# Kernel tuning notes

Measured on AMD Instinct MI355X. Metric: run time of the kernel, lower is better.

The kernel has to match this reference:

```python
import jax, jax.numpy as jnp
import numpy as np

N_NODES = 100000
N_EDGES = 1600000
D = 64
NUM_GROUPS = 2


def setup_inputs() -> dict:
    key = jax.random.key(0)
    k_h, k_ws, k_wg, k_src, k_dst, k_grp = jax.random.split(key, 6)
    h = jax.random.normal(k_h, (N_NODES, D), dtype=jnp.float32)
    # nn.Linear(in, out, bias=False) weights have shape [out, in]
    W_self = jax.random.normal(k_ws, (D, D), dtype=jnp.float32) * (1.0 / np.sqrt(D))
    W_groups = jax.random.normal(k_wg, (NUM_GROUPS, D, D), dtype=jnp.float32) * (1.0 / np.sqrt(D))
    src = jax.random.randint(k_src, (N_EDGES,), 0, N_NODES, dtype=jnp.int32)
    dst = jax.random.randint(k_dst, (N_EDGES,), 0, N_NODES, dtype=jnp.int32)
    group_labels = jax.random.randint(k_grp, (N_NODES,), 0, NUM_GROUPS, dtype=jnp.int32)
    return {"h": h, "W_self": W_self, "W_groups": W_groups,
            "src": src, "dst": dst, "group_labels": group_labels}


def reference(h, W_self, W_groups, src, dst, group_labels):
    # h: [N, d_in]; W_self: [d_out, d_in]; W_groups: [G, d_out, d_in]
    # Edge list (src, dst) replaces the DGL graph; message m_e = h[src_e],
    # transformed by W_groups[group[src_e]], scatter-added into dst_e.
    n_nodes = h.shape[0]
    num_groups = W_groups.shape[0]

    h_self = h @ W_self.T                       # [N, d_out]

    h_src = jnp.take(h, src, axis=0)            # [E, d_in] edge gather
    g_src = jnp.take(group_labels, src, axis=0)  # [E]

    h_agg = jnp.zeros((n_nodes, W_groups.shape[1]), dtype=h.dtype)
    for i in range(num_groups):  # small fixed loop over groups
        masked = jnp.where((g_src == i)[:, None], h_src, 0.0)  # [E, d_in]
        # Linearity lets us aggregate first, then transform (same math as
        # transforming each message then scatter_add, but far less compute).
        seg = jax.ops.segment_sum(masked, dst, num_segments=n_nodes)  # [N, d_in]
        h_agg = h_agg + seg @ W_groups[i].T      # [N, d_out]

    return h_self + h_agg
```

## Files before the change

### kernel.cpp

```cpp
#include <hip/hip_runtime.h>

#define N_NODES 100000
#define N_EDGES 1600000
#define D 64
#define NB 784
#define NR 8
#define CAPB_R 384
#define NGB 3125
#define LCAP 64
#define LSTR 68
#define SRC_MASK 0x1FFFF
#define NBB 782
#define NTC 12500
#define ZB ((u32)(N_NODES * 128))

typedef unsigned int u32;
typedef short bfrag8 __attribute__((ext_vector_type(8)));
typedef float f32x4 __attribute__((ext_vector_type(4)));
typedef float f32x2 __attribute__((ext_vector_type(2)));


__device__ inline u32 pk_bf16(float lo, float hi) {
    u32 a = __float_as_uint(lo);
    a = (a + 0x7fffu + ((a >> 16) & 1u)) >> 16;
    u32 b = __float_as_uint(hi);
    b = (b + 0x7fffu + ((b >> 16) & 1u)) & 0xffff0000u;
    return a | b;
}

__global__ __launch_bounds__(256) void prep(const float* __restrict__ h,
                                            const float* __restrict__ W_self,
                                            const float* __restrict__ W_groups,
                                            const int* __restrict__ src,
                                            const int* __restrict__ dst,
                                            const int* __restrict__ grp,
                                            int* __restrict__ bcnt,
                                            int* __restrict__ buckets,
                                            u32* __restrict__ h_bf,
                                            u32* __restrict__ Wc) {
    __shared__ int hist[NB];
    __shared__ int gbase[NB];
    const int tid = threadIdx.x;
    const int bx = blockIdx.x;

    if (bx < NBB) {
        const int r = bx & (NR - 1);
        for (int b = tid; b < NB; b += 256) hist[b] = 0;
        __syncthreads();

        int ent[8], bkt[8], rnk[8];
        const int e0 = bx * 2048;
#pragma unroll
        for (int i = 0; i < 8; ++i) {
            int e = e0 + tid + i * 256;
            if (e < N_EDGES) {
                int s = src[e], d = dst[e];
                int g = grp[s];
                bkt[i] = d >> 7;
                ent[i] = s | (g << 17) | ((d & 127) << 18);
                rnk[i] = atomicAdd(&hist[bkt[i]], 1);
            } else {
                bkt[i] = -1;
            }
        }
        __syncthreads();
        for (int b = tid; b < NB; b += 256) {
            int hc = hist[b];
            gbase[b] = hc ? atomicAdd(&bcnt[b * NR + r], hc) : 0;
        }
        __syncthreads();
#pragma unroll
        for (int i = 0; i < 8; ++i) {
            if (bkt[i] >= 0) {
                int pos = gbase[bkt[i]] + rnk[i];
                if (pos < CAPB_R)
                    buckets[(bkt[i] * NR + r) * CAPB_R + pos] = ent[i];
            }
        }
    } else if (bx < NBB + NTC) {
        int i = (bx - NBB) * 256 + tid;
        float2 v = reinterpret_cast<const float2*>(h)[i];
        h_bf[i] = pk_bf16(v.x, v.y);
    } else {
        for (int idx = tid; idx < 6144; idx += 256) {
            int j = idx / 96, kk = idx - j * 96;
            int k = kk * 2;
            float lo, hi;
            if (k < 64)       { lo = W_self[j * 64 + k];          hi = W_self[j * 64 + k + 1]; }
            else if (k < 128) { lo = W_groups[j * 64 + k - 64];   hi = W_groups[j * 64 + k - 63]; }
            else              { lo = W_groups[4096 + j * 64 + k - 128];
                                hi = W_groups[4096 + j * 64 + k - 127]; }
            Wc[j * 96 + kk] = pk_bf16(lo, hi);
        }
        if (tid < 32) h_bf[N_NODES * 32 + tid] = 0u;
    }
}

__global__ __launch_bounds__(256, 4) void gather_gemm(const u32* __restrict__ h_bf,
                                                      const int* __restrict__ bcnt,
                                                      const int* __restrict__ buckets,
                                                      const u32* __restrict__ Wc,
                                                      float* __restrict__ out) {
    __shared__ __align__(16) int lcsr[32 * LSTR];
    __shared__ int cntg[64];

    const int tid = threadIdx.x;
    const int cb = blockIdx.x >> 2;
    const int sub = blockIdx.x & 3;
    const int nbase = cb * 128 + sub * 32;
    if (nbase >= N_NODES) return;

    if (tid < 64) cntg[tid] = 0;
    {
        const int4 zb4 = make_int4((int)ZB, (int)ZB, (int)ZB, (int)ZB);
        int4* l4 = reinterpret_cast<int4*>(lcsr);
        for (int t = tid; t < (32 * LSTR) / 4; t += 256) l4[t] = zb4;
    }
    __syncthreads();

    {
        int cns[NR];
        const int4 cA = *reinterpret_cast<const int4*>(bcnt + cb * NR);
        const int4 cB = *reinterpret_cast<const int4*>(bcnt + cb * NR + 4);
        cns[0] = min(cA.x, CAPB_R); cns[1] = min(cA.y, CAPB_R);
        cns[2] = min(cA.z, CAPB_R); cns[3] = min(cA.w, CAPB_R);
        cns[4] = min(cB.x, CAPB_R); cns[5] = min(cB.y, CAPB_R);
        cns[6] = min(cB.z, CAPB_R); cns[7] = min(cB.w, CAPB_R);

        int eA[NR], eB[NR];
#pragma unroll
        for (int r = 0; r < NR; ++r) {
            const int* bp = buckets + (cb * NR + r) * CAPB_R;
            eA[r] = (tid < cns[r])       ? bp[tid]       : -1;
            eB[r] = (tid + 256 < cns[r]) ? bp[tid + 256] : -1;
        }
#pragma unroll
        for (int r = 0; r < NR; ++r) {
            int e = eA[r];
            if (e >= 0 && ((e >> 23) & 3) == sub) {
                int nl = (e >> 18) & 31;
                int g  = (e >> 17) & 1;
                u32 off = ((u32)e & SRC_MASK) << 7;
                int idx = atomicAdd(&cntg[g * 32 + nl], 1);
                int pos = g ? (LCAP - 1 - idx) : idx;
                if (idx < LCAP) lcsr[nl * LSTR + pos] = (int)off;
            }
        }
#pragma unroll
        for (int r = 0; r < NR; ++r) {
            int e = eB[r];
            if (e >= 0 && ((e >> 23) & 3) == sub) {
                int nl = (e >> 18) & 31;
                int g  = (e >> 17) & 1;
                u32 off = ((u32)e & SRC_MASK) << 7;
                int idx = atomicAdd(&cntg[g * 32 + nl], 1);
                int pos = g ? (LCAP - 1 - idx) : idx;
                if (idx < LCAP) lcsr[nl * LSTR + pos] = (int)off;
            }
        }
    }
    __syncthreads();

    const int wave = tid >> 6;
    const int lane = tid & 63;
    const int half = lane >> 5;
    const u32 c4 = (u32)((lane & 31) * 4);
    const char* hb = (const char*)h_bf;

    for (int qp = 0; qp < 2; ++qp) {
        int bse[4], c0[4], c1[4];
#pragma unroll
        for (int t = 0; t < 4; ++t) {
            const int nl = wave * 8 + qp + t * 2;
            bse[t] = nl * LSTR;
            c0[t] = min(cntg[nl], LCAP);
            c1[t] = min(cntg[32 + nl], LCAP);
        }
        f32x2 s0[4], s1[4];
#pragma unroll
        for (int t = 0; t < 4; ++t) {
            s0[t] = (f32x2){0.f, 0.f};
            s1[t] = (f32x2){0.f, 0.f};
        }

        {
            const int m0 = max(max(c0[0], c0[1]), max(c0[2], c0[3]));
            for (int w = 0; w * 8 < m0; ++w) {
                const int i0 = w * 8 + 4 * half;
                int4 sv[4];
#pragma unroll
                for (int t = 0; t < 4; ++t)
                    sv[t] = *reinterpret_cast<const int4*>(&lcsr[bse[t] + i0]);
                u32 x[16];
#pragma unroll
                for (int t = 0; t < 4; ++t) {
                    x[t * 4 + 0] = *(const u32*)(hb + ((u32)sv[t].x + c4));
                    x[t * 4 + 1] = *(const u32*)(hb + ((u32)sv[t].y + c4));
                    x[t * 4 + 2] = *(const u32*)(hb + ((u32)sv[t].z + c4));
                    x[t * 4 + 3] = *(const u32*)(hb + ((u32)sv[t].w + c4));
                }
#pragma unroll
                for (int t = 0; t < 4; ++t) {
#pragma unroll
                    for (int k = 0; k < 4; ++k) {
                        u32 v = x[t * 4 + k];
                        f32x2 tv;
                        tv.x = __uint_as_float(v << 16);
                        tv.y = __uint_as_float(v & 0xffff0000u);
                        s0[t] += tv;
                    }
                }
            }
        }

        {
            const int m1 = max(max(c1[0], c1[1]), max(c1[2], c1[3]));
            for (int w = 0; w * 8 < m1; ++w) {
                const int ro = (LCAP - 4) - w * 8 - 4 * half;
                int4 sv[4];
#pragma unroll
                for (int t = 0; t < 4; ++t)
                    sv[t] = *reinterpret_cast<const int4*>(&lcsr[bse[t] + ro]);
                u32 x[16];
#pragma unroll
                for (int t = 0; t < 4; ++t) {
                    x[t * 4 + 0] = *(const u32*)(hb + ((u32)sv[t].x + c4));
                    x[t * 4 + 1] = *(const u32*)(hb + ((u32)sv[t].y + c4));
                    x[t * 4 + 2] = *(const u32*)(hb + ((u32)sv[t].z + c4));
                    x[t * 4 + 3] = *(const u32*)(hb + ((u32)sv[t].w + c4));
                }
#pragma unroll
                for (int t = 0; t < 4; ++t) {
#pragma unroll
                    for (int k = 0; k < 4; ++k) {
                        u32 v = x[t * 4 + k];
                        f32x2 tv;
                        tv.x = __uint_as_float(v << 16);
                        tv.y = __uint_as_float(v & 0xffff0000u);
                        s1[t] += tv;
                    }
                }
            }
        }

#pragma unroll
        for (int t = 0; t < 4; ++t) {
            s0[t].x += __shfl_xor(s0[t].x, 32, 64);
            s0[t].y += __shfl_xor(s0[t].y, 32, 64);
            s1[t].x += __shfl_xor(s1[t].x, 32, 64);
            s1[t].y += __shfl_xor(s1[t].y, 32, 64);
        }

        if (half == 0) {
            const int c = lane & 31;
#pragma unroll
            for (int t = 0; t < 4; ++t) {
                lcsr[bse[t] + c]      = (int)pk_bf16(s0[t].x, s0[t].y);
                lcsr[bse[t] + 32 + c] = (int)pk_bf16(s1[t].x, s1[t].y);
            }
        }
    }
    __syncthreads();

    const int m = lane & 15;
    const int quad = lane >> 4;
    const int rowh = wave & 1;
    const int jth = wave >> 1;
    const int nl16 = rowh * 16 + m;
    const int arow = nbase + nl16;

    union Cvt { uint4 u; bfrag8 s; };
    bfrag8 a[6];
    const u32* ap = h_bf + (size_t)arow * 32 + quad * 4;
#pragma unroll
    for (int ks = 0; ks < 2; ++ks) {
        Cvt cv2;
        cv2.u = *reinterpret_cast<const uint4*>(ap + ks * 16);
        a[ks] = cv2.s;
    }
#pragma unroll
    for (int ks = 2; ks < 6; ++ks) {
        Cvt cv2;
        cv2.u = *reinterpret_cast<const uint4*>(&lcsr[nl16 * LSTR + (ks - 2) * 16 + quad * 4]);
        a[ks] = cv2.s;
    }

    f32x4 acc[2];
#pragma unroll
    for (int jj = 0; jj < 2; ++jj) acc[jj] = (f32x4){0.f, 0.f, 0.f, 0.f};

    const u32* wp = Wc + (size_t)m * 96 + quad * 4;
#pragma unroll
    for (int ks = 0; ks < 6; ++ks) {
#pragma unroll
        for (int jj = 0; jj < 2; ++jj) {
            Cvt cw;
            cw.u = *reinterpret_cast<const uint4*>(wp + (jth * 2 + jj) * 1536 + ks * 16);
            acc[jj] = __builtin_amdgcn_mfma_f32_16x16x32_bf16(a[ks], cw.s, acc[jj], 0, 0, 0);
        }
    }

    const int rbase = nbase + rowh * 16 + quad * 4;
#pragma unroll
    for (int jj = 0; jj < 2; ++jj) {
#pragma unroll
        for (int r2 = 0; r2 < 4; ++r2) {
            out[(size_t)(rbase + r2) * 64 + (jth * 2 + jj) * 16 + m] = acc[jj][r2];
        }
    }
}

extern "C" void kernel_launch(void* const* d_in, const int* in_sizes, int n_in,
                              void* d_out, int out_size, void* d_ws, size_t ws_size,
                              hipStream_t stream) {
    const float* h        = (const float*)d_in[0];
    const float* W_self   = (const float*)d_in[1];
    const float* W_groups = (const float*)d_in[2];
    const int*   src      = (const int*)d_in[3];
    const int*   dst      = (const int*)d_in[4];
    const int*   grp      = (const int*)d_in[5];
    float*       out      = (float*)d_out;

    int* bcnt    = (int*)d_ws;
    int* buckets = bcnt + 8192;
    u32* h_bf    = (u32*)(buckets + NB * NR * CAPB_R);
    u32* Wc      = h_bf + (size_t)N_NODES * 32 + 32;

    hipMemsetAsync(bcnt, 0, NB * NR * sizeof(int), stream);

    prep<<<NBB + NTC + 1, 256, 0, stream>>>(h, W_self, W_groups, src, dst, grp,
                                            bcnt, buckets, h_bf, Wc);
    gather_gemm<<<NGB, 256, 0, stream>>>(h_bf, bcnt, buckets, Wc, out);
}
```

Baseline: 169.7 us.

## Use 512-thread blocks covering 64 nodes, halving bucket re-reads in gather_gemm

Each gather_gemm block now processes 64 destination nodes with 512 threads instead of 32 nodes with 256 threads, so each coarse bucket is scanned by two blocks rather than four. This cuts redundant global reads of the bucket arrays and the per-block filtering work. In exchange, blocks use twice the LDS, have larger sync domains, and need bounds guards on the last partial block.

```diff
diff --git a/kernel.cpp b/kernel.cpp
--- a/kernel.cpp
+++ b/kernel.cpp
@@ -6,7 +6,6 @@
 #define NB 784
 #define NR 8
 #define CAPB_R 384
-#define NGB 3125
 #define LCAP 64
 #define LSTR 68
 #define SRC_MASK 0x1FFFF
@@ -96,25 +95,25 @@
     }
 }
 
-__global__ __launch_bounds__(256, 4) void gather_gemm(const u32* __restrict__ h_bf,
+__global__ __launch_bounds__(512, 4) void gather_gemm(const u32* __restrict__ h_bf,
                                                       const int* __restrict__ bcnt,
                                                       const int* __restrict__ buckets,
                                                       const u32* __restrict__ Wc,
                                                       float* __restrict__ out) {
-    __shared__ __align__(16) int lcsr[32 * LSTR];
-    __shared__ int cntg[64];
+    __shared__ __align__(16) int lcsr[64 * LSTR];
+    __shared__ int cntg[128];
 
     const int tid = threadIdx.x;
-    const int cb = blockIdx.x >> 2;
-    const int sub = blockIdx.x & 3;
-    const int nbase = cb * 128 + sub * 32;
+    const int cb = blockIdx.x >> 1;
+    const int sub = blockIdx.x & 1;
+    const int nbase = cb * 128 + sub * 64;
     if (nbase >= N_NODES) return;
 
-    if (tid < 64) cntg[tid] = 0;
+    if (tid < 128) cntg[tid] = 0;
     {
         const int4 zb4 = make_int4((int)ZB, (int)ZB, (int)ZB, (int)ZB);
         int4* l4 = reinterpret_cast<int4*>(lcsr);
-        for (int t = tid; t < (32 * LSTR) / 4; t += 256) l4[t] = zb4;
+        for (int t = tid; t < (64 * LSTR) / 4; t += 512) l4[t] = zb4;
     }
     __syncthreads();
 
@@ -127,33 +126,20 @@
         cns[4] = min(cB.x, CAPB_R); cns[5] = min(cB.y, CAPB_R);
         cns[6] = min(cB.z, CAPB_R); cns[7] = min(cB.w, CAPB_R);
 
-        int eA[NR], eB[NR];
+        int eA[NR];
 #pragma unroll
         for (int r = 0; r < NR; ++r) {
             const int* bp = buckets + (cb * NR + r) * CAPB_R;
-            eA[r] = (tid < cns[r])       ? bp[tid]       : -1;
-            eB[r] = (tid + 256 < cns[r]) ? bp[tid + 256] : -1;
+            eA[r] = (tid < cns[r]) ? bp[tid] : -1;
         }
 #pragma unroll
         for (int r = 0; r < NR; ++r) {
             int e = eA[r];
-            if (e >= 0 && ((e >> 23) & 3) == sub) {
-                int nl = (e >> 18) & 31;
+            if (e >= 0 && ((e >> 24) & 1) == sub) {
+                int nl = (e >> 18) & 63;
                 int g  = (e >> 17) & 1;
                 u32 off = ((u32)e & SRC_MASK) << 7;
-                int idx = atomicAdd(&cntg[g * 32 + nl], 1);
-                int pos = g ? (LCAP - 1 - idx) : idx;
-                if (idx < LCAP) lcsr[nl * LSTR + pos] = (int)off;
-            }
-        }
-#pragma unroll
-        for (int r = 0; r < NR; ++r) {
-            int e = eB[r];
-            if (e >= 0 && ((e >> 23) & 3) == sub) {
-                int nl = (e >> 18) & 31;
-                int g  = (e >> 17) & 1;
-                u32 off = ((u32)e & SRC_MASK) << 7;
-                int idx = atomicAdd(&cntg[g * 32 + nl], 1);
+                int idx = atomicAdd(&cntg[g * 64 + nl], 1);
                 int pos = g ? (LCAP - 1 - idx) : idx;
                 if (idx < LCAP) lcsr[nl * LSTR + pos] = (int)off;
             }
@@ -174,7 +160,7 @@
             const int nl = wave * 8 + qp + t * 2;
             bse[t] = nl * LSTR;
             c0[t] = min(cntg[nl], LCAP);
-            c1[t] = min(cntg[32 + nl], LCAP);
+            c1[t] = min(cntg[64 + nl], LCAP);
         }
         f32x2 s0[4], s1[4];
 #pragma unroll
@@ -264,14 +250,15 @@
 
     const int m = lane & 15;
     const int quad = lane >> 4;
-    const int rowh = wave & 1;
-    const int jth = wave >> 1;
-    const int nl16 = rowh * 16 + m;
-    const int arow = nbase + nl16;
+    const int rowh = wave & 3;
+    const int jth = wave >> 2;
+    const int nl64 = rowh * 16 + m;
+    const int arow = nbase + nl64;
+    const int ar = (arow < N_NODES) ? arow : (N_NODES - 1);
 
     union Cvt { uint4 u; bfrag8 s; };
     bfrag8 a[6];
-    const u32* ap = h_bf + (size_t)arow * 32 + quad * 4;
+    const u32* ap = h_bf + (size_t)ar * 32 + quad * 4;
 #pragma unroll
     for (int ks = 0; ks < 2; ++ks) {
         Cvt cv2;
@@ -281,7 +268,7 @@
 #pragma unroll
     for (int ks = 2; ks < 6; ++ks) {
         Cvt cv2;
-        cv2.u = *reinterpret_cast<const uint4*>(&lcsr[nl16 * LSTR + (ks - 2) * 16 + quad * 4]);
+        cv2.u = *reinterpret_cast<const uint4*>(&lcsr[nl64 * LSTR + (ks - 2) * 16 + quad * 4]);
         a[ks] = cv2.s;
     }
 
@@ -305,7 +292,9 @@
     for (int jj = 0; jj < 2; ++jj) {
 #pragma unroll
         for (int r2 = 0; r2 < 4; ++r2) {
-            out[(size_t)(rbase + r2) * 64 + (jth * 2 + jj) * 16 + m] = acc[jj][r2];
+            int n = rbase + r2;
+            if (n < N_NODES)
+                out[(size_t)n * 64 + (jth * 2 + jj) * 16 + m] = acc[jj][r2];
         }
     }
 }
@@ -330,5 +319,5 @@
 
     prep<<<NBB + NTC + 1, 256, 0, stream>>>(h, W_self, W_groups, src, dst, grp,
                                             bcnt, buckets, h_bf, Wc);
-    gather_gemm<<<NGB, 256, 0, stream>>>(h_bf, bcnt, buckets, Wc, out);
+    gather_gemm<<<NB * 2, 512, 0, stream>>>(h_bf, bcnt, buckets, Wc, out);
 }
```

New measurement: 172.2 us. Within noise of the previous version (+1.5%).
